# Performance work log

Measured on AMD Instinct MI355X. Metric: run time of the kernel, lower is better.

Reference implementation:

```python
import jax, jax.numpy as jnp
import numpy as np

INPUT_SIZE = 1024
HIDDEN_SIZE = 1024
W_RANK = 64
U_RANK = 64
BATCH = 32768


def setup_inputs() -> dict:
    key = jax.random.key(0)
    ks = jax.random.split(key, 16)
    p = lambda k, shape: 0.1 * jax.random.normal(k, shape, dtype=jnp.float32)
    return {
        "x": jax.random.normal(ks[0], (BATCH, INPUT_SIZE), dtype=jnp.float32),
        "h": jax.random.normal(ks[1], (BATCH, HIDDEN_SIZE), dtype=jnp.float32),
        "W": p(ks[2], (INPUT_SIZE, W_RANK)),
        "W1": p(ks[3], (W_RANK, HIDDEN_SIZE)),
        "W2": p(ks[4], (W_RANK, HIDDEN_SIZE)),
        "W3": p(ks[5], (W_RANK, HIDDEN_SIZE)),
        "U": p(ks[6], (HIDDEN_SIZE, U_RANK)),
        "U1": p(ks[7], (U_RANK, HIDDEN_SIZE)),
        "U2": p(ks[8], (U_RANK, HIDDEN_SIZE)),
        "U3": p(ks[9], (U_RANK, HIDDEN_SIZE)),
        "U1_diag": p(ks[10], (HIDDEN_SIZE,)),
        "U2_diag": p(ks[11], (HIDDEN_SIZE,)),
        "U3_diag": p(ks[12], (HIDDEN_SIZE,)),
        "bias_r": jnp.ones((1, HIDDEN_SIZE), dtype=jnp.float32),
        "bias_gate": jnp.ones((1, HIDDEN_SIZE), dtype=jnp.float32),
        "bias_update": jnp.ones((1, HIDDEN_SIZE), dtype=jnp.float32),
    }


def reference(x, h, W, W1, W2, W3, U, U1, U2, U3,
              U1_diag, U2_diag, U3_diag, bias_r, bias_gate, bias_update):
    # Low-rank projections shared across gates (matches torch matmul order)
    xW = x @ W          # [B, wRank]
    hU = h @ U          # [B, uRank]
    wVal1 = xW @ W1
    wVal2 = xW @ W2
    wVal3 = xW @ W3
    uVal1 = hU @ U1
    uVal2 = hU @ U2
    r = jax.nn.sigmoid(wVal1 + uVal1 + h * U1_diag + bias_r)
    z = jax.nn.sigmoid(wVal2 + uVal2 + h * U2_diag + bias_gate)
    rh = r * h
    matVal_c = wVal3 + (rh @ U) @ U3 + rh * U3_diag
    c_tilda = jnp.tanh(matVal_c + bias_update)
    h_next = z * h + (1.0 - z) * c_tilda
    return h_next
```

## Files before the change

### kernel.cpp

```cpp
#include <hip/hip_runtime.h>
#include <hip/hip_bf16.h>


typedef __attribute__((ext_vector_type(8))) short short8;
typedef __attribute__((ext_vector_type(4))) float f32x4;
typedef __attribute__((ext_vector_type(4))) float f4;

#define WS_UT   65536
#define WS_P1T  131072
#define WS_P2T  262144
#define WS_P3T  393216
#define WS_A12  524288
#define WS_RHU  4718592

__device__ __forceinline__ short f2bf(float f) {
  unsigned u = __builtin_bit_cast(unsigned, f);
  u += 0x7FFFu + ((u >> 16) & 1u);
  return (short)(u >> 16);
}
__device__ __forceinline__ short8 cvt8(f4 a, f4 b) {
  short8 r;
#pragma unroll
  for (int j = 0; j < 4; ++j) { r[j] = f2bf(a[j]); r[4 + j] = f2bf(b[j]); }
  return r;
}
__device__ __forceinline__ f32x4 mfma16(short8 a, short8 b, f32x4 c) {
  return __builtin_amdgcn_mfma_f32_16x16x32_bf16(a, b, c, 0, 0, 0);
}
__device__ __forceinline__ short8 ldg8(const short* p) {
  return *reinterpret_cast<const short8*>(p);
}
__device__ __forceinline__ f4 ldf4(const float* p) {
  return *reinterpret_cast<const f4*>(p);
}

__device__ __forceinline__ void cp16(void* l, const void* g) {
  __builtin_amdgcn_global_load_lds(
      (const __attribute__((address_space(1))) void*)g,
      (__attribute__((address_space(3))) void*)l, 16, 0, 0);
}
#define VWAIT(N) do { asm volatile("s_waitcnt vmcnt(" #N ")" ::: "memory"); \
                      __builtin_amdgcn_sched_barrier(0); } while (0)

__device__ __forceinline__ short8 rd128s(const short* b, int row, int col) {
  return *reinterpret_cast<const short8*>(b + row * 128 + (col ^ ((row & 7) << 3)));
}
__device__ __forceinline__ void wr128s(short* b, int row, int col8, short8 v) {
  *reinterpret_cast<short8*>(b + row * 128 + (col8 ^ ((row & 7) << 3))) = v;
}
__device__ __forceinline__ void wr64(short* b, int row, int col, short v) {
  b[row * 64 + (col ^ ((row & 7) << 3))] = v;
}
__device__ __forceinline__ short8 rd64(const short* b, int row, int col) {
  return *reinterpret_cast<const short8*>(b + row * 64 + (col ^ ((row & 7) << 3)));
}

#define LOG2E 1.4426950408889634f
__device__ __forceinline__ float sigm_f(float v) {
  return __builtin_amdgcn_rcpf(1.f + __builtin_amdgcn_exp2f(-v * LOG2E));
}
__device__ __forceinline__ float tanh_f(float v) {
  float t = __builtin_amdgcn_exp2f(v * (2.f * LOG2E));
  return 1.f - 2.f * __builtin_amdgcn_rcpf(t + 1.f);
}

__global__ void prep_kernel(const float* __restrict__ W,  const float* __restrict__ W1,
                            const float* __restrict__ W2, const float* __restrict__ W3,
                            const float* __restrict__ U,  const float* __restrict__ U1,
                            const float* __restrict__ U2, const float* __restrict__ U3,
                            short* __restrict__ ws) {
  int i = blockIdx.x * blockDim.x + threadIdx.x;
  float v;
  if (i < 65536) {
    int n = i >> 10, k = i & 1023;
    v = W[k * 64 + n];
  } else if (i < 131072) {
    int j = i - 65536;
    int n = j >> 10, k = j & 1023;
    v = U[k * 64 + n];
  } else {
    int j = i - 131072;
    int sel = j >> 17;
    int jj = j & 131071;
    int n = jj >> 7, k = jj & 127;
    const float* Wk = sel == 0 ? W1 : sel == 1 ? W2 : W3;
    const float* Uk = sel == 0 ? U1 : sel == 1 ? U2 : U3;
    v = (k < 64) ? Wk[k * 1024 + n] : Uk[(k - 64) * 1024 + n];
  }
  ws[i] = f2bf(v);
}

__global__ __launch_bounds__(256, 4) void k1_a12(
    const float* __restrict__ x, const float* __restrict__ h,
    const short* __restrict__ ws, short* __restrict__ A12) {
  __shared__ __align__(16) float sS[4][4][16 * 32];

  const int tid = threadIdx.x;
  const int w = tid >> 6, l = tid & 63, l15 = l & 15, lg = l >> 4;
  const int m = w >> 1, half = w & 1;
  const int sr = blockIdx.x * 32 + half * 16;
  const float* src = m ? h : x;
  const short* Bt  = ws + m * WS_UT;

  const int srow = l >> 3;
  const int slin = (l & 7) * 16;

  auto STAGE = [&](int c, int b) {
#pragma unroll
    for (int i = 0; i < 2; ++i) {
      int r = i * 8 + srow;
      int kb = slin ^ ((r & 7) << 4);
      cp16((char*)&sS[b][w][0] + i * 1024,
           (const char*)(src + (size_t)(sr + r) * 1024 + c * 32) + kb);
    }
  };
  auto WLOAD = [&](int c, short8* bw) {
#pragma unroll
    for (int cf = 0; cf < 4; ++cf)
      bw[cf] = ldg8(Bt + (size_t)(cf * 16 + l15) * 1024 + c * 32 + lg * 8);
  };

  f32x4 acc[4] = {};
  short8 bwb[4][4];
  WLOAD(0, bwb[0]); STAGE(0, 0);
  WLOAD(1, bwb[1]); STAGE(1, 1);
  WLOAD(2, bwb[2]); STAGE(2, 2);

#pragma unroll
  for (int c = 0; c < 32; ++c) {
    if (c <= 28) {
      WLOAD(c + 3, bwb[(c + 3) & 3]);
      STAGE(c + 3, (c + 3) & 3);
      VWAIT(18);
    } else if (c == 29) {
      VWAIT(12);
    } else if (c == 30) {
      VWAIT(6);
    } else {
      VWAIT(0);
    }
    const char* Bb = (const char*)&sS[c & 3][w][0];
    const int s = (l15 & 7) << 4;
    f4 pa = *(const f4*)(Bb + l15 * 128 + ((lg * 32) ^ s));
    f4 pb = *(const f4*)(Bb + l15 * 128 + ((lg * 32 + 16) ^ s));
    short8 av = cvt8(pa, pb);
    const short8* bw = bwb[c & 3];
#pragma unroll
    for (int cf = 0; cf < 4; ++cf) acc[cf] = mfma16(av, bw[cf], acc[cf]);
  }

#pragma unroll
  for (int cf = 0; cf < 4; ++cf)
#pragma unroll
    for (int j = 0; j < 4; ++j)
      A12[(size_t)(sr + lg * 4 + j) * 128 + m * 64 + cf * 16 + l15] = f2bf(acc[cf][j]);
}

__global__ __launch_bounds__(256, 4) void k23_rhu(
    const float* __restrict__ h, const float* __restrict__ u1d,
    const float* __restrict__ biasR,
    const short* __restrict__ ws, const short* __restrict__ A12,
    short* __restrict__ rhU) {
  const short* Ut  = ws + WS_UT;
  const short* P1t = ws + WS_P1T;
  __shared__ __align__(16) short sT[4][2][16 * 64];
  __shared__ __align__(16) float sRed[2][2][16 * 64];

  const int tid = threadIdx.x;
  const int w   = tid >> 6, l = tid & 63, l15 = l & 15, lg = l >> 4;
  const int s   = w >> 1;
  const int ch  = w & 1;
  const int sr  = blockIdx.x * 32 + s * 16;

  short8 a12[4];
#pragma unroll
  for (int k0 = 0; k0 < 4; ++k0)
    a12[k0] = ldg8(A12 + (size_t)(sr + l15) * 128 + k0 * 32 + lg * 8);

  f32x4 accU[4] = {};
#pragma unroll 1
  for (int tt = 0; tt < 8; ++tt) {
    const int n0 = ch * 512 + tt * 64;

    float hv[4][4];
#pragma unroll
    for (int cf = 0; cf < 4; ++cf)
#pragma unroll
      for (int j = 0; j < 4; ++j)
        hv[cf][j] = h[(size_t)(sr + lg * 4 + j) * 1024 + n0 + cf * 16 + l15];

    f32x4 accR[4] = {};
#pragma unroll
    for (int k0 = 0; k0 < 4; ++k0)
#pragma unroll
      for (int cf = 0; cf < 4; ++cf)
        accR[cf] = mfma16(a12[k0],
            ldg8(P1t + (size_t)(n0 + cf * 16 + l15) * 128 + k0 * 32 + lg * 8),
            accR[cf]);

    short* sw = &sT[w][tt & 1][0];
#pragma unroll
    for (int cf = 0; cf < 4; ++cf) {
      const int cc = n0 + cf * 16 + l15;
      const float d1 = u1d[cc], b_r = biasR[cc];
#pragma unroll
      for (int j = 0; j < 4; ++j) {
        float rv = sigm_f(accR[cf][j] + hv[cf][j] * d1 + b_r);
        wr64(sw, lg * 4 + j, cf * 16 + l15, f2bf(rv * hv[cf][j]));
      }
    }
    short8 arh0 = rd64(sw, l15, lg * 8);
    short8 arh1 = rd64(sw, l15, 32 + lg * 8);
#pragma unroll
    for (int cf = 0; cf < 4; ++cf)
      accU[cf] = mfma16(arh0,
          ldg8(Ut + (size_t)(cf * 16 + l15) * 1024 + n0 + lg * 8), accU[cf]);
#pragma unroll
    for (int cf = 0; cf < 4; ++cf)
      accU[cf] = mfma16(arh1,
          ldg8(Ut + (size_t)(cf * 16 + l15) * 1024 + n0 + 32 + lg * 8), accU[cf]);
  }

  {
    float* fT = &sRed[s][ch][0];
#pragma unroll
    for (int cf = 0; cf < 4; ++cf)
#pragma unroll
      for (int j = 0; j < 4; ++j) {
        int row = lg * 4 + j, col = cf * 16 + l15;
        fT[row * 64 + (col ^ ((row & 7) << 2))] = accU[cf][j];
      }
  }
  __syncthreads();
  if (ch == 0) {
    const float* f0 = &sRed[s][0][0];
    const float* f1 = &sRed[s][1][0];
#pragma unroll
    for (int cf = 0; cf < 4; ++cf)
#pragma unroll
      for (int j = 0; j < 4; ++j) {
        int row = lg * 4 + j, col = cf * 16 + l15;
        int idx = row * 64 + (col ^ ((row & 7) << 2));
        rhU[(size_t)(sr + row) * 64 + col] = f2bf(f0[idx] + f1[idx]);
      }
  }
}

__global__ __launch_bounds__(256, 2) void k4_out(
    const float* __restrict__ h,
    const float* __restrict__ u1d, const float* __restrict__ u2d,
    const float* __restrict__ u3d,
    const float* __restrict__ biasR, const float* __restrict__ biasZ,
    const float* __restrict__ biasU,
    const short* __restrict__ ws, const short* __restrict__ A12,
    const short* __restrict__ rhU, float* __restrict__ out) {
  __shared__ __align__(16) short sB1[64 * 128], sB2[64 * 128], sB3[64 * 128];
  __shared__ __align__(16) float hS[2][4][16 * 64];

  const int tid = threadIdx.x;
  const int w = tid >> 6, l = tid & 63, l15 = l & 15, lg = l >> 4;
  const int ct = blockIdx.x & 15, rc = blockIdx.x >> 4;
  const int n0 = ct * 64;

#pragma unroll
  for (int mat = 0; mat < 3; ++mat) {
    const short* srcw = (mat == 0) ? (ws + WS_P1T) : (mat == 1) ? (ws + WS_P2T) : (ws + WS_P3T);
    short* dst = (mat == 0) ? sB1 : (mat == 1) ? sB2 : sB3;
#pragma unroll
    for (int i = 0; i < 4; ++i) {
      int id = tid + i * 256;
      int row = id >> 4, gc = id & 15;
      wr128s(dst, row, gc * 8, ldg8(srcw + (size_t)(n0 + row) * 128 + gc * 8));
    }
  }
  float d1_[4], d2_[4], d3_[4], br_[4], bz_[4], bu_[4];
#pragma unroll
  for (int cf = 0; cf < 4; ++cf) {
    const int cc = n0 + cf * 16 + l15;
    d1_[cf] = u1d[cc]; d2_[cf] = u2d[cc]; d3_[cf] = u3d[cc];
    br_[cf] = biasR[cc]; bz_[cf] = biasZ[cc]; bu_[cf] = biasU[cc];
  }
  __syncthreads();

  const int srow = l >> 4;
  const int slin = (l & 15) * 16;
  auto STAGE = [&](int rnd, int b) {
    const int sb = rc * 512 + rnd * 64 + w * 16;
#pragma unroll
    for (int i = 0; i < 4; ++i) {
      int r = i * 4 + srow;
      int kb = slin ^ ((r & 7) << 4);
      cp16((char*)&hS[b][w][0] + i * 1024,
           (const char*)(h + (size_t)(sb + r) * 1024 + n0) + kb);
    }
  };

  STAGE(0, 0);
#pragma unroll 1
  for (int rnd = 0; rnd < 8; ++rnd) {
    const int sr = rc * 512 + rnd * 64 + w * 16;
    short8 a12[4], arhu[2];
#pragma unroll
    for (int k0 = 0; k0 < 4; ++k0)
      a12[k0] = ldg8(A12 + (size_t)(sr + l15) * 128 + k0 * 32 + lg * 8);
#pragma unroll
    for (int kk = 0; kk < 2; ++kk)
      arhu[kk] = ldg8(rhU + (size_t)(sr + l15) * 64 + kk * 32 + lg * 8);
    if (rnd < 7) { STAGE(rnd + 1, (rnd + 1) & 1); VWAIT(4); }
    else         { VWAIT(0); }
    const char* H = (const char*)&hS[rnd & 1][w][0];

    float hv[4][4];
#pragma unroll
    for (int cf = 0; cf < 4; ++cf)
#pragma unroll
      for (int j = 0; j < 4; ++j) {
        int rr = lg * 4 + j;
        hv[cf][j] = *(const float*)(H + rr * 256 + ((cf * 64 + l15 * 4) ^ ((rr & 7) << 4)));
      }

    f32x4 aR[4] = {}, aZ[4] = {}, aC[4] = {};
#pragma unroll
    for (int k0 = 0; k0 < 4; ++k0) {
      const short8 a3 = (k0 < 2) ? a12[k0] : arhu[k0 - 2];
#pragma unroll
      for (int cf = 0; cf < 4; ++cf) {
        aR[cf] = mfma16(a12[k0], rd128s(sB1, cf * 16 + l15, k0 * 32 + lg * 8), aR[cf]);
        aZ[cf] = mfma16(a12[k0], rd128s(sB2, cf * 16 + l15, k0 * 32 + lg * 8), aZ[cf]);
        aC[cf] = mfma16(a3,      rd128s(sB3, cf * 16 + l15, k0 * 32 + lg * 8), aC[cf]);
      }
    }
#pragma unroll
    for (int cf = 0; cf < 4; ++cf) {
      const int cc = n0 + cf * 16 + l15;
#pragma unroll
      for (int j = 0; j < 4; ++j) {
        const size_t gi = (size_t)(sr + lg * 4 + j) * 1024 + cc;
        const float hvj = hv[cf][j];
        float rv = sigm_f(aR[cf][j] + hvj * d1_[cf] + br_[cf]);
        float zv = sigm_f(aZ[cf][j] + hvj * d2_[cf] + bz_[cf]);
        float cv = tanh_f(aC[cf][j] + rv * hvj * d3_[cf] + bu_[cf]);
        out[gi] = zv * hvj + (1.f - zv) * cv;
      }
    }
  }
}

extern "C" void kernel_launch(void* const* d_in, const int* in_sizes, int n_in,
                              void* d_out, int out_size, void* d_ws, size_t ws_size,
                              hipStream_t stream) {
  const float* x   = (const float*)d_in[0];
  const float* h   = (const float*)d_in[1];
  const float* W   = (const float*)d_in[2];
  const float* W1  = (const float*)d_in[3];
  const float* W2  = (const float*)d_in[4];
  const float* W3  = (const float*)d_in[5];
  const float* U   = (const float*)d_in[6];
  const float* U1  = (const float*)d_in[7];
  const float* U2  = (const float*)d_in[8];
  const float* U3  = (const float*)d_in[9];
  const float* u1d = (const float*)d_in[10];
  const float* u2d = (const float*)d_in[11];
  const float* u3d = (const float*)d_in[12];
  const float* bR  = (const float*)d_in[13];
  const float* bZ  = (const float*)d_in[14];
  const float* bU  = (const float*)d_in[15];
  short* ws  = (short*)d_ws;
  short* A12 = ws + WS_A12;
  short* rhU = ws + WS_RHU;

  prep_kernel<<<2048, 256, 0, stream>>>(W, W1, W2, W3, U, U1, U2, U3, ws);
  k1_a12<<<1024, 256, 0, stream>>>(x, h, ws, A12);
  k23_rhu<<<1024, 256, 0, stream>>>(h, u1d, bR, ws, A12, rhU);
  k4_out<<<1024, 256, 0, stream>>>(h, u1d, u2d, u3d, bR, bZ, bU, ws, A12, rhU, (float*)d_out);
}
```

Measured before the change: 254.4 us.

## Stage full projection weight in LDS and stream activations via register ring

k1_a12 now loads the whole 64x1024 bf16 projection matrix (W or U) into a 128KB swizzled LDS buffer once per block. Each block handles 128 rows of one input instead of splitting x/h across waves, so the weight is no longer re-fetched from global memory for every chunk. Activations are read straight from global into an 8-deep register ring instead of going through LDS async copies. The cost is one block per CU (512 threads, large LDS) with a serialized weight-load prologue, and higher register pressure from the ring.

```diff
diff --git a/kernel.cpp b/kernel.cpp
--- a/kernel.cpp
+++ b/kernel.cpp
@@ -90,63 +90,66 @@
   ws[i] = f2bf(v);
 }
 
-__global__ __launch_bounds__(256, 4) void k1_a12(
+__global__ __launch_bounds__(512, 1) void k1_a12(
     const float* __restrict__ x, const float* __restrict__ h,
     const short* __restrict__ ws, short* __restrict__ A12) {
-  __shared__ __align__(16) float sS[4][4][16 * 32];
+  __shared__ __align__(16) short sW[64 * 1024];
 
   const int tid = threadIdx.x;
   const int w = tid >> 6, l = tid & 63, l15 = l & 15, lg = l >> 4;
-  const int m = w >> 1, half = w & 1;
-  const int sr = blockIdx.x * 32 + half * 16;
+  const int m  = blockIdx.x & 1;
+  const int rc = blockIdx.x >> 1;
+  const int sr = rc * 128 + w * 16;
   const float* src = m ? h : x;
   const short* Bt  = ws + m * WS_UT;
 
-  const int srow = l >> 3;
-  const int slin = (l & 7) * 16;
-
-  auto STAGE = [&](int c, int b) {
-#pragma unroll
-    for (int i = 0; i < 2; ++i) {
-      int r = i * 8 + srow;
-      int kb = slin ^ ((r & 7) << 4);
-      cp16((char*)&sS[b][w][0] + i * 1024,
-           (const char*)(src + (size_t)(sr + r) * 1024 + c * 32) + kb);
-    }
+#pragma unroll
+  for (int rnd = 0; rnd < 16; ++rnd) {
+    const int byte = rnd * 8192 + tid * 16;
+    const int row  = byte >> 11;
+    const int col  = byte & 2047;
+    const int scol = col ^ ((row & 7) << 4);
+    cp16((char*)sW + byte, (const char*)(Bt + row * 1024) + scol);
+  }
+  VWAIT(0);
+  __syncthreads();
+
+  auto rdW = [&](int row, int kcol) {
+    const int byte = row * 2048 + ((kcol * 2) ^ ((row & 7) << 4));
+    return *reinterpret_cast<const short8*>((const char*)sW + byte);
   };
-  auto WLOAD = [&](int c, short8* bw) {
-#pragma unroll
-    for (int cf = 0; cf < 4; ++cf)
-      bw[cf] = ldg8(Bt + (size_t)(cf * 16 + l15) * 1024 + c * 32 + lg * 8);
-  };
+
+  const float* xr = src + (size_t)(sr + l15) * 1024 + lg * 8;
+
+  f4 ring[8][2];
+#pragma unroll
+  for (int i = 0; i < 8; ++i) {
+    ring[i][0] = ldf4(xr + i * 32);
+    ring[i][1] = ldf4(xr + i * 32 + 4);
+  }
 
   f32x4 acc[4] = {};
-  short8 bwb[4][4];
-  WLOAD(0, bwb[0]); STAGE(0, 0);
-  WLOAD(1, bwb[1]); STAGE(1, 1);
-  WLOAD(2, bwb[2]); STAGE(2, 2);
-
 #pragma unroll
   for (int c = 0; c < 32; ++c) {
-    if (c <= 28) {
-      WLOAD(c + 3, bwb[(c + 3) & 3]);
-      STAGE(c + 3, (c + 3) & 3);
-      VWAIT(18);
-    } else if (c == 29) {
-      VWAIT(12);
-    } else if (c == 30) {
-      VWAIT(6);
-    } else {
-      VWAIT(0);
-    }
-    const char* Bb = (const char*)&sS[c & 3][w][0];
-    const int s = (l15 & 7) << 4;
-    f4 pa = *(const f4*)(Bb + l15 * 128 + ((lg * 32) ^ s));
-    f4 pb = *(const f4*)(Bb + l15 * 128 + ((lg * 32 + 16) ^ s));
-    short8 av = cvt8(pa, pb);
-    const short8* bw = bwb[c & 3];
-#pragma unroll
-    for (int cf = 0; cf < 4; ++cf) acc[cf] = mfma16(av, bw[cf], acc[cf]);
+    if (c < 25)      VWAIT(14);
+    else if (c == 25) VWAIT(12);
+    else if (c == 26) VWAIT(10);
+    else if (c == 27) VWAIT(8);
+    else if (c == 28) VWAIT(6);
+    else if (c == 29) VWAIT(4);
+    else if (c == 30) VWAIT(2);
+    else              VWAIT(0);
+
+    short8 av = cvt8(ring[c & 7][0], ring[c & 7][1]);
+    const int kcol = c * 32 + lg * 8;
+#pragma unroll
+    for (int cf = 0; cf < 4; ++cf)
+      acc[cf] = mfma16(av, rdW(cf * 16 + l15, kcol), acc[cf]);
+
+    if (c < 24) {
+      ring[c & 7][0] = ldf4(xr + (c + 8) * 32);
+      ring[c & 7][1] = ldf4(xr + (c + 8) * 32 + 4);
+    }
   }
 
 #pragma unroll
@@ -370,7 +373,7 @@
   short* rhU = ws + WS_RHU;
 
   prep_kernel<<<2048, 256, 0, stream>>>(W, W1, W2, W3, U, U1, U2, U3, ws);
-  k1_a12<<<1024, 256, 0, stream>>>(x, h, ws, A12);
+  k1_a12<<<512, 512, 0, stream>>>(x, h, ws, A12);
   k23_rhu<<<1024, 256, 0, stream>>>(h, u1d, bR, ws, A12, rhU);
   k4_out<<<1024, 256, 0, stream>>>(h, u1d, u2d, u3d, bR, bZ, bU, ws, A12, rhU, (float*)d_out);
 }
```

New measurement: 214.9 us. 15.5% less time.
